# Kernel tuning notes

Measured on AMD Instinct MI355X. Metric: run time of the kernel, lower is better.

Reference implementation:

```python
import jax, jax.numpy as jnp
import numpy as np

N = 50000
NEG_SLOPE = 0.2  # PyG GATConv default leaky_relu slope


def _gat_layer(x, src, dst, W, a_s, a_d, b):
    # x: [N, Fin]; W: [Fin, H*C]; a_s, a_d: [H, C]; b: [C]
    H, C = a_s.shape
    xp = (x @ W).reshape(N, H, C)                      # projected node features per head
    alpha_s = jnp.einsum('nhc,hc->nh', xp, a_s)        # [N, H]
    alpha_d = jnp.einsum('nhc,hc->nh', xp, a_d)        # [N, H]
    e = jax.nn.leaky_relu(alpha_s[src] + alpha_d[dst], NEG_SLOPE)  # [E, H]
    # segment softmax over incoming edges of each dst node
    m = jax.ops.segment_max(e, dst, num_segments=N)
    m = jnp.where(jnp.isfinite(m), m, 0.0)
    p = jnp.exp(e - jax.lax.stop_gradient(m)[dst])
    denom = jax.ops.segment_sum(p, dst, num_segments=N)
    alpha = p / denom[dst]                             # [E, H]
    # scatter-aggregate messages
    out = jax.ops.segment_sum(alpha[:, :, None] * xp[src], dst, num_segments=N)  # [N, H, C]
    return out.mean(axis=1) + b                        # concat=False -> mean over heads


def setup_inputs() -> dict:
    key = jax.random.key(0)
    ks = jax.random.split(key, 16)
    IN, HID, OUT, H = 128, 64, 40, 4
    E = 800000
    x = jax.random.normal(ks[0], (N, IN), dtype=jnp.float32)
    edge_index = jax.random.randint(ks[1], (2, E), 0, N, dtype=jnp.int64)

    def mk(kw, ka, fin, fout):
        s = 1.0 / np.sqrt(fin)
        W = jax.random.normal(kw, (fin, H * fout), dtype=jnp.float32) * s
        a_s = jax.random.normal(ka, (H, fout), dtype=jnp.float32) * 0.1
        a_d = jax.random.normal(jax.random.fold_in(ka, 1), (H, fout), dtype=jnp.float32) * 0.1
        b = jnp.zeros((fout,), dtype=jnp.float32)
        return W, a_s, a_d, b

    W1, as1, ad1, b1 = mk(ks[2], ks[3], IN, HID)
    W2, as2, ad2, b2 = mk(ks[4], ks[5], HID, HID)
    W3, as3, ad3, b3 = mk(ks[6], ks[7], HID, OUT)
    return dict(x=x, edge_index=edge_index,
                W1=W1, as1=as1, ad1=ad1, b1=b1,
                W2=W2, as2=as2, ad2=ad2, b2=b2,
                W3=W3, as3=as3, ad3=ad3, b3=b3)


def reference(x, edge_index, W1, as1, ad1, b1, W2, as2, ad2, b2, W3, as3, ad3, b3):
    # PyG GATConv adds self-loops by default
    loop = jnp.arange(N, dtype=edge_index.dtype)
    src = jnp.concatenate([edge_index[0], loop])
    dst = jnp.concatenate([edge_index[1], loop])
    h = jax.nn.relu(_gat_layer(x, src, dst, W1, as1, ad1, b1))   # dropout is identity in eval
    h = jax.nn.relu(_gat_layer(h, src, dst, W2, as2, ad2, b2))
    h = jax.nn.relu(_gat_layer(h, src, dst, W3, as3, ad3, b3))
    return jax.nn.log_softmax(h, axis=-1)
```

## Files before the change

### kernel.cpp

```cpp
#include <hip/hip_runtime.h>
#include <math.h>

#define NNODES 50000
#define NEG_SLOPE 0.2f

typedef unsigned short ushort8v __attribute__((ext_vector_type(8)));
typedef unsigned short ushort4v __attribute__((ext_vector_type(4)));
typedef short short8v __attribute__((ext_vector_type(8)));
typedef float f32x4 __attribute__((ext_vector_type(4)));
typedef float f32x2 __attribute__((ext_vector_type(2)));

__device__ __forceinline__ unsigned short f2bf(float f){
    unsigned u = __float_as_uint(f);
    u += 0x7fff + ((u >> 16) & 1);
    return (unsigned short)(u >> 16);
}

__device__ __forceinline__ void emit_wa(const float* __restrict__ W, const float* __restrict__ a_s,
                                        const float* __restrict__ a_d, unsigned short* __restrict__ Wt,
                                        int Kin, int C, int id){
    const int n = id / Kin, k = id - n * Kin;
    float v = 0.f;
    if(n < 8){
        const int hh = n & 3;
        const float* av = (n < 4) ? a_s : a_d;
        for(int c = 0; c < C; c++) v += W[(size_t)k * (4 * C) + hh * C + c] * av[hh * C + c];
    }
    Wt[id] = f2bf(v);
}

__device__ __forceinline__ void emit_wc(const float* __restrict__ W, unsigned short* __restrict__ Wt,
                                        int Kin, int C, int id){
    const int c = id / (4 * Kin);
    const int hk = id - c * (4 * Kin);
    const int h = hk / Kin, k = hk - h * Kin;
    const float v = (c < C) ? W[(size_t)k * (4 * C) + h * C + c] * 0.25f : 0.f;
    Wt[id] = f2bf(v);
}

__global__ void initprep_kernel(const unsigned long long* __restrict__ e, int* __restrict__ flag,
                                int* __restrict__ deg, int N,
                                const float* __restrict__ x, unsigned short* __restrict__ xbf, int X4,
                                const float* __restrict__ W1, const float* __restrict__ as1, const float* __restrict__ ad1,
                                const float* __restrict__ W2, const float* __restrict__ as2, const float* __restrict__ ad2,
                                const float* __restrict__ W3, const float* __restrict__ as3, const float* __restrict__ ad3,
                                unsigned short* __restrict__ Wa1, unsigned short* __restrict__ Wa2,
                                unsigned short* __restrict__ Wa3, unsigned short* __restrict__ Wc1,
                                unsigned short* __restrict__ Wc2, unsigned short* __restrict__ Wc3){
    if(blockIdx.x == 0 && threadIdx.x < 64){
        const unsigned long long v = e[threadIdx.x];
        const unsigned long long mask = __ballot(v >= (1ULL << 32));
        if(threadIdx.x == 0) *flag = (mask == 0ULL) ? 1 : 0;
    }
    int id = blockIdx.x * blockDim.x + threadIdx.x;
    if(id < N) deg[id] = 0;
    if(id < X4){
        const float4 v = *(const float4*)&x[(size_t)id * 4];
        ushort4v o;
        o[0] = f2bf(v.x); o[1] = f2bf(v.y); o[2] = f2bf(v.z); o[3] = f2bf(v.w);
        *(ushort4v*)&xbf[(size_t)id * 4] = o;
        return;
    }
    id -= X4;
    if(id < 16 * 128){ emit_wa(W1, as1, ad1, Wa1, 128, 64, id); return; }
    id -= 16 * 128;
    if(id < 16 * 64){ emit_wa(W2, as2, ad2, Wa2, 64, 64, id); return; }
    id -= 16 * 64;
    if(id < 16 * 64){ emit_wa(W3, as3, ad3, Wa3, 64, 40, id); return; }
    id -= 16 * 64;
    if(id < 64 * 512){ emit_wc(W1, Wc1, 128, 64, id); return; }
    id -= 64 * 512;
    if(id < 64 * 256){ emit_wc(W2, Wc2, 64, 64, id); return; }
    id -= 64 * 256;
    if(id < 48 * 256){ emit_wc(W3, Wc3, 64, 40, id); }
}

__global__ void hist_kernel(const void* __restrict__ e, const int* __restrict__ flag,
                            int* __restrict__ deg, int E){
    const int i = blockIdx.x * blockDim.x + threadIdx.x;
    if(i < E){
        const int d = (*flag) ? (int)((const long long*)e)[E + i] : ((const int*)e)[E + i];
        atomicAdd(&deg[d], 1);
    }
}

__global__ __launch_bounds__(512) void scan1_kernel(const int* __restrict__ deg,
                                                    int* __restrict__ excl,
                                                    int* __restrict__ bsum, int n){
    __shared__ int sh[512];
    const int t = threadIdx.x;
    const int gid = blockIdx.x * 512 + t;
    const int v = (gid < n) ? deg[gid] : 0;
    sh[t] = v;
    __syncthreads();
    for(int off = 1; off < 512; off <<= 1){
        const int add = (t >= off) ? sh[t - off] : 0;
        __syncthreads();
        sh[t] += add;
        __syncthreads();
    }
    if(gid < n) excl[gid] = sh[t] - v;
    if(t == 511) bsum[blockIdx.x] = sh[511];
}

__global__ __launch_bounds__(128) void scan2_kernel(int* __restrict__ bsum, int nb){
    __shared__ int sh[128];
    const int t = threadIdx.x;
    const int v = (t < nb) ? bsum[t] : 0;
    sh[t] = v;
    __syncthreads();
    for(int off = 1; off < 128; off <<= 1){
        const int add = (t >= off) ? sh[t - off] : 0;
        __syncthreads();
        sh[t] += add;
        __syncthreads();
    }
    if(t < nb) bsum[t] = sh[t] - v;
}

__global__ void scan3_kernel(const int* __restrict__ excl, const int* __restrict__ bsum,
                             int* __restrict__ row_ptr, int* __restrict__ cursor,
                             int n, int E){
    const int gid = blockIdx.x * blockDim.x + threadIdx.x;
    if(gid < n){
        const int r = excl[gid] + bsum[gid >> 9];
        row_ptr[gid] = r;
        cursor[gid] = r;
    }
    if(gid == 0) row_ptr[n] = E;
}

__global__ void scatter_kernel(const void* __restrict__ e, const int* __restrict__ flag,
                               int* __restrict__ cursor, int* __restrict__ col, int E){
    const int i = blockIdx.x * blockDim.x + threadIdx.x;
    if(i < E){
        int s, d;
        if(*flag){ s = (int)((const long long*)e)[i]; d = (int)((const long long*)e)[E + i]; }
        else     { s = ((const int*)e)[i];            d = ((const int*)e)[E + i]; }
        const int pos = atomicAdd(&cursor[d], 1);
        col[pos] = s;
    }
}

template<int K>
__global__ __launch_bounds__(256) void agemm_kernel(const unsigned short* __restrict__ A,
                                                    const unsigned short* __restrict__ Wa,
                                                    float* __restrict__ ea, float* __restrict__ ed,
                                                    int M){
    const int lane = threadIdx.x & 63;
    const int wave = threadIdx.x >> 6;
    const int quad = lane >> 4;
    const int l16 = lane & 15;
    const int bm = blockIdx.x * 64;
    const int m = min(bm + wave * 16 + l16, M - 1);
    f32x4 acc = {0,0,0,0};
    #pragma unroll
    for(int k0 = 0; k0 < K; k0 += 32){
        const short8v a = *(const short8v*)&A[(size_t)m * K + k0 + quad * 8];
        const short8v b = *(const short8v*)&Wa[(size_t)l16 * K + k0 + quad * 8];
        acc = __builtin_amdgcn_mfma_f32_16x16x32_bf16(a, b, acc, 0, 0, 0);
    }
    if(l16 < 8){
        const int h = l16 & 3;
        float* dst = (l16 < 4) ? ea : ed;
        const int rbase = bm + wave * 16 + quad * 4;
        #pragma unroll
        for(int r = 0; r < 4; r++){
            const int row = rbase + r;
            if(row < M){
                const float v = acc[r];
                *(f32x2*)&dst[(size_t)row * 8 + 2 * h] = (f32x2){__expf(v), __expf(NEG_SLOPE * v)};
            }
        }
    }
}

template<int K, int NC, bool FINAL, bool ALPHA>
__global__ __launch_bounds__(256) void fused_kernel(const unsigned short* __restrict__ X,
                                                    const int* __restrict__ row_ptr,
                                                    const int* __restrict__ col,
                                                    const float* __restrict__ ea,
                                                    const float* __restrict__ ed,
                                                    const unsigned short* __restrict__ Bt,
                                                    const float* __restrict__ bias,
                                                    void* __restrict__ outv,
                                                    const unsigned short* __restrict__ Wa,
                                                    float* __restrict__ ea_o,
                                                    float* __restrict__ ed_o){
    constexpr int KC = 4 * K;
    constexpr int CPL = K / 16;
    constexpr int PAIRS = CPL / 2;
    constexpr int LSTR = KC + 8;
    __shared__ unsigned short lg[16][LSTR];
    __shared__ unsigned short lh[ALPHA ? 16 : 1][72];
    __shared__ float lo[FINAL ? 16 : 1][48];

    const int lane = threadIdx.x & 63;
    const int wave = threadIdx.x >> 6;
    const int slot = lane >> 4;
    const int pos  = lane & 15;
    const int nb   = blockIdx.x * 16;

    #pragma unroll 1
    for(int i = 0; i < 4; i++){
        const int row16 = wave * 4 + i;
        const int n = nb + row16;
        const int rs = row_ptr[n], re = row_ptr[n + 1];
        const int T = re - rs + 1;
        const float4 edA = *(const float4*)&ed[(size_t)n * 8];
        const float4 edB = *(const float4*)&ed[(size_t)n * 8 + 4];

        f32x2 acc[4][PAIRS];
        #pragma unroll
        for(int h = 0; h < 4; h++)
            #pragma unroll
            for(int p = 0; p < PAIRS; p++) acc[h][p] = (f32x2){0.f, 0.f};
        float dnm[4] = {0.f, 0.f, 0.f, 0.f};

        auto body = [&](int e){
            const int s = (e < re) ? col[e] : n;
            const float4 eaA = *(const float4*)&ea[(size_t)s * 8];
            const float4 eaB = *(const float4*)&ea[(size_t)s * 8 + 4];
            const float w0 = fmaxf(eaA.x * edA.x, eaA.y * edA.y);
            const float w1 = fmaxf(eaA.z * edA.z, eaA.w * edA.w);
            const float w2 = fmaxf(eaB.x * edB.x, eaB.y * edB.y);
            const float w3 = fmaxf(eaB.z * edB.z, eaB.w * edB.w);
            dnm[0] += w0; dnm[1] += w1; dnm[2] += w2; dnm[3] += w3;
            unsigned u[PAIRS];
            if constexpr(PAIRS == 2){
                const uint2 t2 = *(const uint2*)&X[(size_t)s * K + pos * CPL];
                u[0] = t2.x; u[1] = t2.y;
            } else {
                const uint4 t4 = *(const uint4*)&X[(size_t)s * K + pos * CPL];
                u[0] = t4.x; u[1] = t4.y; u[2] = t4.z; u[3] = t4.w;
            }
            #pragma unroll
            for(int p = 0; p < PAIRS; p++){
                const f32x2 v = {__uint_as_float(u[p] << 16), __uint_as_float(u[p] & 0xffff0000u)};
                acc[0][p] += (f32x2){w0, w0} * v;
                acc[1][p] += (f32x2){w1, w1} * v;
                acc[2][p] += (f32x2){w2, w2} * v;
                acc[3][p] += (f32x2){w3, w3} * v;
            }
        };

        int k = 0;
        for(; k + 8 <= T; k += 8){ body(rs + k + slot); body(rs + k + 4 + slot); }
        for(; k + 4 <= T; k += 4){ body(rs + k + slot); }
        if(k < T && slot < T - k){ body(rs + k + slot); }

        #pragma unroll
        for(int msk = 16; msk < 64; msk <<= 1){
            #pragma unroll
            for(int h = 0; h < 4; h++){
                #pragma unroll
                for(int p = 0; p < PAIRS; p++){
                    acc[h][p][0] += __shfl_xor(acc[h][p][0], msk);
                    acc[h][p][1] += __shfl_xor(acc[h][p][1], msk);
                }
                dnm[h] += __shfl_xor(dnm[h], msk);
            }
        }
        if(lane < 16){
            #pragma unroll
            for(int h = 0; h < 4; h++){
                const float sc = 1.f / dnm[h];
                if constexpr(PAIRS == 2){
                    ushort4v o;
                    o[0] = f2bf(acc[h][0][0] * sc); o[1] = f2bf(acc[h][0][1] * sc);
                    o[2] = f2bf(acc[h][1][0] * sc); o[3] = f2bf(acc[h][1][1] * sc);
                    *(ushort4v*)&lg[row16][h * K + pos * CPL] = o;
                } else {
                    ushort8v o;
                    #pragma unroll
                    for(int p = 0; p < 4; p++){
                        o[2*p]   = f2bf(acc[h][p][0] * sc);
                        o[2*p+1] = f2bf(acc[h][p][1] * sc);
                    }
                    *(ushort8v*)&lg[row16][h * K + pos * CPL] = o;
                }
            }
        }
    }
    __syncthreads();

    if constexpr(!FINAL){
        f32x4 acc4 = {0, 0, 0, 0};
        const int c = wave * 16 + pos;
        for(int k0 = 0; k0 < KC; k0 += 32){
            const short8v a = *(const short8v*)&lg[pos][k0 + slot * 8];
            const short8v b = *(const short8v*)&Bt[(size_t)c * KC + k0 + slot * 8];
            acc4 = __builtin_amdgcn_mfma_f32_16x16x32_bf16(a, b, acc4, 0, 0, 0);
        }
        unsigned short* out = (unsigned short*)outv;
        const float bc = bias[c];
        #pragma unroll
        for(int r = 0; r < 4; r++){
            const unsigned short hb = f2bf(fmaxf(acc4[r] + bc, 0.f));
            out[(size_t)(nb + slot * 4 + r) * NC + c] = hb;
            if constexpr(ALPHA) lh[slot * 4 + r][c] = hb;
        }
        if constexpr(ALPHA){
            __syncthreads();
            if(wave == 0){
                f32x4 a4 = {0, 0, 0, 0};
                #pragma unroll
                for(int k0 = 0; k0 < 64; k0 += 32){
                    const short8v a = *(const short8v*)&lh[pos][k0 + slot * 8];
                    const short8v b = *(const short8v*)&Wa[(size_t)pos * 64 + k0 + slot * 8];
                    a4 = __builtin_amdgcn_mfma_f32_16x16x32_bf16(a, b, a4, 0, 0, 0);
                }
                if(pos < 8){
                    const int h = pos & 3;
                    float* dst = (pos < 4) ? ea_o : ed_o;
                    #pragma unroll
                    for(int r = 0; r < 4; r++){
                        const int row = nb + slot * 4 + r;
                        const float v = a4[r];
                        *(f32x2*)&dst[(size_t)row * 8 + 2 * h] = (f32x2){__expf(v), __expf(NEG_SLOPE * v)};
                    }
                }
            }
        }
    } else {
        if(wave < 3){
            f32x4 acc4 = {0, 0, 0, 0};
            const int c = wave * 16 + pos;
            for(int k0 = 0; k0 < KC; k0 += 32){
                const short8v a = *(const short8v*)&lg[pos][k0 + slot * 8];
                const short8v b = *(const short8v*)&Bt[(size_t)c * KC + k0 + slot * 8];
                acc4 = __builtin_amdgcn_mfma_f32_16x16x32_bf16(a, b, acc4, 0, 0, 0);
            }
            const bool valid = c < 40;
            const float bc = valid ? bias[c] : 0.f;
            #pragma unroll
            for(int r = 0; r < 4; r++)
                lo[slot * 4 + r][c] = valid ? fmaxf(acc4[r] + bc, 0.f) : -INFINITY;
        }
        __syncthreads();
        const int r  = threadIdx.x >> 4;
        const int cc = threadIdx.x & 15;
        const float o0 = lo[r][cc];
        const float o1 = lo[r][cc + 16];
        const float o2 = lo[r][cc + 32];
        float mx = fmaxf(fmaxf(o0, o1), o2);
        #pragma unroll
        for(int off = 1; off < 16; off <<= 1) mx = fmaxf(mx, __shfl_xor(mx, off));
        float se = __expf(o0 - mx) + __expf(o1 - mx) + ((o2 > -INFINITY) ? __expf(o2 - mx) : 0.f);
        #pragma unroll
        for(int off = 1; off < 16; off <<= 1) se += __shfl_xor(se, off);
        const float lz = mx + logf(se);
        float* out = (float*)outv;
        const size_t rb = (size_t)(nb + r) * 40;
        out[rb + cc] = o0 - lz;
        out[rb + cc + 16] = o1 - lz;
        if(cc < 8) out[rb + cc + 32] = o2 - lz;
    }
}

extern "C" void kernel_launch(void* const* d_in, const int* in_sizes, int n_in,
                              void* d_out, int out_size, void* d_ws, size_t ws_size,
                              hipStream_t stream){
    const int N = NNODES;
    const int E = in_sizes[1] / 2;

    const float* x   = (const float*)d_in[0];
    const float* W1  = (const float*)d_in[2];
    const float* as1 = (const float*)d_in[3];
    const float* ad1 = (const float*)d_in[4];
    const float* b1  = (const float*)d_in[5];
    const float* W2  = (const float*)d_in[6];
    const float* as2 = (const float*)d_in[7];
    const float* ad2 = (const float*)d_in[8];
    const float* b2  = (const float*)d_in[9];
    const float* W3  = (const float*)d_in[10];
    const float* as3 = (const float*)d_in[11];
    const float* ad3 = (const float*)d_in[12];
    const float* b3  = (const float*)d_in[13];

    char* ws = (char*)d_ws;
    size_t off = 0;
    auto alloc = [&](size_t bytes) -> void* {
        void* p = ws + off;
        off = (off + bytes + 255) & ~(size_t)255;
        return p;
    };
    int*   flag    = (int*)  alloc(4);
    int*   row_ptr = (int*)  alloc((size_t)(N + 1) * 4);
    int*   colv    = (int*)  alloc((size_t)E * 4);
    int*   cursor  = (int*)  alloc((size_t)N * 4);
    int*   deg     = (int*)  alloc((size_t)N * 4);
    int*   excl    = (int*)  alloc((size_t)N * 4);
    int*   bsum    = (int*)  alloc(128 * 4);
    unsigned short* xbf = (unsigned short*)alloc((size_t)N * 128 * 2);
    unsigned short* Wa1 = (unsigned short*)alloc(16 * 128 * 2);
    unsigned short* Wa2 = (unsigned short*)alloc(16 * 64 * 2);
    unsigned short* Wa3 = (unsigned short*)alloc(16 * 64 * 2);
    unsigned short* Wc1 = (unsigned short*)alloc((size_t)64 * 512 * 2);
    unsigned short* Wc2 = (unsigned short*)alloc((size_t)64 * 256 * 2);
    unsigned short* Wc3 = (unsigned short*)alloc((size_t)48 * 256 * 2);
    float* eav0 = (float*)alloc((size_t)N * 8 * 4);
    float* edv0 = (float*)alloc((size_t)N * 8 * 4);
    float* eav1 = (float*)alloc((size_t)N * 8 * 4);
    float* edv1 = (float*)alloc((size_t)N * 8 * 4);
    unsigned short* h1  = (unsigned short*)alloc((size_t)N * 64 * 2);
    unsigned short* h2  = (unsigned short*)alloc((size_t)N * 64 * 2);
    (void)ws_size;

    const void* eraw = d_in[1];

    const int X4 = N * 128 / 4;
    const int prepTotal = X4 + 16*128 + 16*64 + 16*64 + 64*512 + 64*256 + 48*256;
    initprep_kernel<<<(prepTotal + 255) / 256, 256, 0, stream>>>(
        (const unsigned long long*)eraw, flag, deg, N, x, xbf, X4,
        W1, as1, ad1, W2, as2, ad2, W3, as3, ad3,
        Wa1, Wa2, Wa3, Wc1, Wc2, Wc3);

    hist_kernel<<<(E + 255) / 256, 256, 0, stream>>>(eraw, flag, deg, E);
    const int nbScan = (N + 511) / 512;
    scan1_kernel<<<nbScan, 512, 0, stream>>>(deg, excl, bsum, N);
    scan2_kernel<<<1, 128, 0, stream>>>(bsum, nbScan);
    scan3_kernel<<<(N + 255) / 256, 256, 0, stream>>>(excl, bsum, row_ptr, cursor, N, E);
    scatter_kernel<<<(E + 255) / 256, 256, 0, stream>>>(eraw, flag, cursor, colv, E);

    const int mBlocks = (N + 63) / 64;
    const int fBlocks = N / 16;

    agemm_kernel<128><<<mBlocks, 256, 0, stream>>>(xbf, Wa1, eav0, edv0, N);

    fused_kernel<128, 64, false, true><<<fBlocks, 256, 0, stream>>>(
        xbf, row_ptr, colv, eav0, edv0, Wc1, b1, h1, Wa2, eav1, edv1);

    fused_kernel<64, 64, false, true><<<fBlocks, 256, 0, stream>>>(
        h1, row_ptr, colv, eav1, edv1, Wc2, b2, h2, Wa3, eav0, edv0);

    fused_kernel<64, 40, true, false><<<fBlocks, 256, 0, stream>>>(
        h2, row_ptr, colv, eav0, edv0, Wc3, b3, d_out, nullptr, nullptr, nullptr);
}
```

Baseline: 419.3 us.

## Use 1024-thread blocks with one wave per node and split-K MFMA reduction

The fused GAT layer kernels move from 256-thread blocks, where each wave looped over four destination nodes, to 1024-thread blocks where each of 16 waves aggregates a single node. The dense projection that follows is split along K across four wave groups, and the partial MFMA results are summed through shared memory. The aim is more parallelism and latency hiding for the irregular neighbor gathers, and less serial GEMM work per wave. The cost is an extra barrier and shared-memory traffic, larger blocks that can limit occupancy under register pressure, and idle waves during the epilogues.

```diff
diff --git a/kernel.cpp b/kernel.cpp
--- a/kernel.cpp
+++ b/kernel.cpp
@@ -176,22 +176,25 @@
 }
 
 template<int K, int NC, bool FINAL, bool ALPHA>
-__global__ __launch_bounds__(256) void fused_kernel(const unsigned short* __restrict__ X,
-                                                    const int* __restrict__ row_ptr,
-                                                    const int* __restrict__ col,
-                                                    const float* __restrict__ ea,
-                                                    const float* __restrict__ ed,
-                                                    const unsigned short* __restrict__ Bt,
-                                                    const float* __restrict__ bias,
-                                                    void* __restrict__ outv,
-                                                    const unsigned short* __restrict__ Wa,
-                                                    float* __restrict__ ea_o,
-                                                    float* __restrict__ ed_o){
+__global__ __launch_bounds__(1024) void fused_kernel(const unsigned short* __restrict__ X,
+                                                     const int* __restrict__ row_ptr,
+                                                     const int* __restrict__ col,
+                                                     const float* __restrict__ ea,
+                                                     const float* __restrict__ ed,
+                                                     const unsigned short* __restrict__ Bt,
+                                                     const float* __restrict__ bias,
+                                                     void* __restrict__ outv,
+                                                     const unsigned short* __restrict__ Wa,
+                                                     float* __restrict__ ea_o,
+                                                     float* __restrict__ ed_o){
     constexpr int KC = 4 * K;
     constexpr int CPL = K / 16;
     constexpr int PAIRS = CPL / 2;
     constexpr int LSTR = KC + 8;
+    constexpr int NT = (NC + 15) / 16;
+    constexpr int KCH = KC / 4;
     __shared__ unsigned short lg[16][LSTR];
+    __shared__ float pt[3][NT][16][20];
     __shared__ unsigned short lh[ALPHA ? 16 : 1][72];
     __shared__ float lo[FINAL ? 16 : 1][48];
 
@@ -201,10 +204,8 @@
     const int pos  = lane & 15;
     const int nb   = blockIdx.x * 16;
 
-    #pragma unroll 1
-    for(int i = 0; i < 4; i++){
-        const int row16 = wave * 4 + i;
-        const int n = nb + row16;
+    {
+        const int n = nb + wave;
         const int rs = row_ptr[n], re = row_ptr[n + 1];
         const int T = re - rs + 1;
         const float4 edA = *(const float4*)&ed[(size_t)n * 8];
@@ -269,7 +270,7 @@
                     ushort4v o;
                     o[0] = f2bf(acc[h][0][0] * sc); o[1] = f2bf(acc[h][0][1] * sc);
                     o[2] = f2bf(acc[h][1][0] * sc); o[3] = f2bf(acc[h][1][1] * sc);
-                    *(ushort4v*)&lg[row16][h * K + pos * CPL] = o;
+                    *(ushort4v*)&lg[wave][h * K + pos * CPL] = o;
                 } else {
                     ushort8v o;
                     #pragma unroll
@@ -277,28 +278,47 @@
                         o[2*p]   = f2bf(acc[h][p][0] * sc);
                         o[2*p+1] = f2bf(acc[h][p][1] * sc);
                     }
-                    *(ushort8v*)&lg[row16][h * K + pos * CPL] = o;
+                    *(ushort8v*)&lg[wave][h * K + pos * CPL] = o;
                 }
             }
         }
     }
     __syncthreads();
 
-    if constexpr(!FINAL){
-        f32x4 acc4 = {0, 0, 0, 0};
-        const int c = wave * 16 + pos;
-        for(int k0 = 0; k0 < KC; k0 += 32){
+    const int t = wave & 3;
+    const int q = wave >> 2;
+    f32x4 acc4 = {0, 0, 0, 0};
+    if(t < NT){
+        const int c = t * 16 + pos;
+        const int kbeg = q * KCH;
+        #pragma unroll
+        for(int k0 = kbeg; k0 < kbeg + KCH; k0 += 32){
             const short8v a = *(const short8v*)&lg[pos][k0 + slot * 8];
             const short8v b = *(const short8v*)&Bt[(size_t)c * KC + k0 + slot * 8];
             acc4 = __builtin_amdgcn_mfma_f32_16x16x32_bf16(a, b, acc4, 0, 0, 0);
         }
-        unsigned short* out = (unsigned short*)outv;
-        const float bc = bias[c];
-        #pragma unroll
-        for(int r = 0; r < 4; r++){
-            const unsigned short hb = f2bf(fmaxf(acc4[r] + bc, 0.f));
-            out[(size_t)(nb + slot * 4 + r) * NC + c] = hb;
-            if constexpr(ALPHA) lh[slot * 4 + r][c] = hb;
+        if(q > 0){
+            #pragma unroll
+            for(int r = 0; r < 4; r++) pt[q - 1][t][slot * 4 + r][pos] = acc4[r];
+        }
+    }
+    __syncthreads();
+
+    if constexpr(!FINAL){
+        if(q == 0){
+            #pragma unroll
+            for(int r = 0; r < 4; r++)
+                acc4[r] += pt[0][t][slot * 4 + r][pos] + pt[1][t][slot * 4 + r][pos]
+                         + pt[2][t][slot * 4 + r][pos];
+            unsigned short* out = (unsigned short*)outv;
+            const int c = t * 16 + pos;
+            const float bc = bias[c];
+            #pragma unroll
+            for(int r = 0; r < 4; r++){
+                const unsigned short hb = f2bf(fmaxf(acc4[r] + bc, 0.f));
+                out[(size_t)(nb + slot * 4 + r) * NC + c] = hb;
+                if constexpr(ALPHA) lh[slot * 4 + r][c] = hb;
+            }
         }
         if constexpr(ALPHA){
             __syncthreads();
@@ -323,38 +343,36 @@
             }
         }
     } else {
-        if(wave < 3){
-            f32x4 acc4 = {0, 0, 0, 0};
-            const int c = wave * 16 + pos;
-            for(int k0 = 0; k0 < KC; k0 += 32){
-                const short8v a = *(const short8v*)&lg[pos][k0 + slot * 8];
-                const short8v b = *(const short8v*)&Bt[(size_t)c * KC + k0 + slot * 8];
-                acc4 = __builtin_amdgcn_mfma_f32_16x16x32_bf16(a, b, acc4, 0, 0, 0);
-            }
-            const bool valid = c < 40;
-            const float bc = valid ? bias[c] : 0.f;
-            #pragma unroll
-            for(int r = 0; r < 4; r++)
-                lo[slot * 4 + r][c] = valid ? fmaxf(acc4[r] + bc, 0.f) : -INFINITY;
+        if(q == 0 && t < NT){
+            #pragma unroll
+            for(int r = 0; r < 4; r++){
+                const float v = acc4[r] + pt[0][t][slot * 4 + r][pos]
+                              + pt[1][t][slot * 4 + r][pos] + pt[2][t][slot * 4 + r][pos];
+                const int c = t * 16 + pos;
+                const bool valid = c < 40;
+                lo[slot * 4 + r][c] = valid ? fmaxf(v + bias[c], 0.f) : -INFINITY;
+            }
         }
         __syncthreads();
-        const int r  = threadIdx.x >> 4;
-        const int cc = threadIdx.x & 15;
-        const float o0 = lo[r][cc];
-        const float o1 = lo[r][cc + 16];
-        const float o2 = lo[r][cc + 32];
-        float mx = fmaxf(fmaxf(o0, o1), o2);
-        #pragma unroll
-        for(int off = 1; off < 16; off <<= 1) mx = fmaxf(mx, __shfl_xor(mx, off));
-        float se = __expf(o0 - mx) + __expf(o1 - mx) + ((o2 > -INFINITY) ? __expf(o2 - mx) : 0.f);
-        #pragma unroll
-        for(int off = 1; off < 16; off <<= 1) se += __shfl_xor(se, off);
-        const float lz = mx + logf(se);
-        float* out = (float*)outv;
-        const size_t rb = (size_t)(nb + r) * 40;
-        out[rb + cc] = o0 - lz;
-        out[rb + cc + 16] = o1 - lz;
-        if(cc < 8) out[rb + cc + 32] = o2 - lz;
+        if(threadIdx.x < 256){
+            const int r  = threadIdx.x >> 4;
+            const int cc = threadIdx.x & 15;
+            const float o0 = lo[r][cc];
+            const float o1 = lo[r][cc + 16];
+            const float o2 = lo[r][cc + 32];
+            float mx = fmaxf(fmaxf(o0, o1), o2);
+            #pragma unroll
+            for(int off = 1; off < 16; off <<= 1) mx = fmaxf(mx, __shfl_xor(mx, off));
+            float se = __expf(o0 - mx) + __expf(o1 - mx) + ((o2 > -INFINITY) ? __expf(o2 - mx) : 0.f);
+            #pragma unroll
+            for(int off = 1; off < 16; off <<= 1) se += __shfl_xor(se, off);
+            const float lz = mx + logf(se);
+            float* out = (float*)outv;
+            const size_t rb = (size_t)(nb + r) * 40;
+            out[rb + cc] = o0 - lz;
+            out[rb + cc + 16] = o1 - lz;
+            if(cc < 8) out[rb + cc + 32] = o2 - lz;
+        }
     }
 }
 
@@ -428,12 +446,12 @@
 
     agemm_kernel<128><<<mBlocks, 256, 0, stream>>>(xbf, Wa1, eav0, edv0, N);
 
-    fused_kernel<128, 64, false, true><<<fBlocks, 256, 0, stream>>>(
+    fused_kernel<128, 64, false, true><<<fBlocks, 1024, 0, stream>>>(
         xbf, row_ptr, colv, eav0, edv0, Wc1, b1, h1, Wa2, eav1, edv1);
 
-    fused_kernel<64, 64, false, true><<<fBlocks, 256, 0, stream>>>(
+    fused_kernel<64, 64, false, true><<<fBlocks, 1024, 0, stream>>>(
         h1, row_ptr, colv, eav1, edv1, Wc2, b2, h2, Wa3, eav0, edv0);
 
-    fused_kernel<64, 40, true, false><<<fBlocks, 256, 0, stream>>>(
+    fused_kernel<64, 40, true, false><<<fBlocks, 1024, 0, stream>>>(
         h2, row_ptr, colv, eav0, edv0, Wc3, b3, d_out, nullptr, nullptr, nullptr);
 }
```

New measurement: 485.6 us. 1.16x slower.

## Precompute per-head projected features then aggregate with one-node-per-wave gather

Applied to the files above, without the earlier changes.

Replaces the aggregate-then-project fused kernel with a GEMM that materialises projected per-head features (plus attention logits) into a bf16 buffer, followed by a gather kernel where each wave handles one node and reads 256-wide projected rows per edge. Edge weights are computed once per edge and staged in LDS, then broadcast across lanes. This removes per-edge multi-head FMA work and the post-aggregation GEMM, but enlarges per-edge gather traffic and adds a write/read of an N×256 intermediate per layer.

```diff
diff --git a/kernel.cpp b/kernel.cpp
--- a/kernel.cpp
+++ b/kernel.cpp
@@ -16,25 +16,22 @@
     return (unsigned short)(u >> 16);
 }
 
-__device__ __forceinline__ void emit_wa(const float* __restrict__ W, const float* __restrict__ a_s,
-                                        const float* __restrict__ a_d, unsigned short* __restrict__ Wt,
-                                        int Kin, int C, int id){
-    const int n = id / Kin, k = id - n * Kin;
+__device__ __forceinline__ void emit_wpt(const float* __restrict__ W, const float* __restrict__ a_s,
+                                         const float* __restrict__ a_d, unsigned short* __restrict__ Wt,
+                                         int Kin, int C, int id){
+    const int j = id / Kin, k = id - j * Kin;
     float v = 0.f;
-    if(n < 8){
-        const int hh = n & 3;
-        const float* av = (n < 4) ? a_s : a_d;
-        for(int c = 0; c < C; c++) v += W[(size_t)k * (4 * C) + hh * C + c] * av[hh * C + c];
-    }
-    Wt[id] = f2bf(v);
-}
-
-__device__ __forceinline__ void emit_wc(const float* __restrict__ W, unsigned short* __restrict__ Wt,
-                                        int Kin, int C, int id){
-    const int c = id / (4 * Kin);
-    const int hk = id - c * (4 * Kin);
-    const int h = hk / Kin, k = hk - h * Kin;
-    const float v = (c < C) ? W[(size_t)k * (4 * C) + h * C + c] * 0.25f : 0.f;
+    if(j < 256){
+        const int h = j >> 6, c = j & 63;
+        v = (c < C) ? W[(size_t)k * (4 * C) + h * C + c] : 0.f;
+    } else {
+        const int n = j - 256;
+        if(n < 8){
+            const int hh = n & 3;
+            const float* av = (n < 4) ? a_s : a_d;
+            for(int c = 0; c < C; c++) v += W[(size_t)k * (4 * C) + hh * C + c] * av[hh * C + c];
+        }
+    }
     Wt[id] = f2bf(v);
 }
 
@@ -44,9 +41,8 @@
                                 const float* __restrict__ W1, const float* __restrict__ as1, const float* __restrict__ ad1,
                                 const float* __restrict__ W2, const float* __restrict__ as2, const float* __restrict__ ad2,
                                 const float* __restrict__ W3, const float* __restrict__ as3, const float* __restrict__ ad3,
-                                unsigned short* __restrict__ Wa1, unsigned short* __restrict__ Wa2,
-                                unsigned short* __restrict__ Wa3, unsigned short* __restrict__ Wc1,
-                                unsigned short* __restrict__ Wc2, unsigned short* __restrict__ Wc3){
+                                unsigned short* __restrict__ WpT1, unsigned short* __restrict__ WpT2,
+                                unsigned short* __restrict__ WpT3){
     if(blockIdx.x == 0 && threadIdx.x < 64){
         const unsigned long long v = e[threadIdx.x];
         const unsigned long long mask = __ballot(v >= (1ULL << 32));
@@ -62,17 +58,11 @@
         return;
     }
     id -= X4;
-    if(id < 16 * 128){ emit_wa(W1, as1, ad1, Wa1, 128, 64, id); return; }
-    id -= 16 * 128;
-    if(id < 16 * 64){ emit_wa(W2, as2, ad2, Wa2, 64, 64, id); return; }
-    id -= 16 * 64;
-    if(id < 16 * 64){ emit_wa(W3, as3, ad3, Wa3, 64, 40, id); return; }
-    id -= 16 * 64;
-    if(id < 64 * 512){ emit_wc(W1, Wc1, 128, 64, id); return; }
-    id -= 64 * 512;
-    if(id < 64 * 256){ emit_wc(W2, Wc2, 64, 64, id); return; }
-    id -= 64 * 256;
-    if(id < 48 * 256){ emit_wc(W3, Wc3, 64, 40, id); }
+    if(id < 272 * 128){ emit_wpt(W1, as1, ad1, WpT1, 128, 64, id); return; }
+    id -= 272 * 128;
+    if(id < 272 * 64){ emit_wpt(W2, as2, ad2, WpT2, 64, 64, id); return; }
+    id -= 272 * 64;
+    if(id < 272 * 64){ emit_wpt(W3, as3, ad3, WpT3, 64, 40, id); }
 }
 
 __global__ void hist_kernel(const void* __restrict__ e, const int* __restrict__ flag,
@@ -143,81 +133,82 @@
 }
 
 template<int K>
-__global__ __launch_bounds__(256) void agemm_kernel(const unsigned short* __restrict__ A,
-                                                    const unsigned short* __restrict__ Wa,
-                                                    float* __restrict__ ea, float* __restrict__ ed,
-                                                    int M){
+__global__ __launch_bounds__(256) void xpgemm_kernel(const unsigned short* __restrict__ A,
+                                                     const unsigned short* __restrict__ Bt,
+                                                     unsigned short* __restrict__ xp,
+                                                     float* __restrict__ ea, float* __restrict__ ed,
+                                                     int M){
+    constexpr int KK = K / 32;
     const int lane = threadIdx.x & 63;
     const int wave = threadIdx.x >> 6;
     const int quad = lane >> 4;
     const int l16 = lane & 15;
     const int bm = blockIdx.x * 64;
     const int m = min(bm + wave * 16 + l16, M - 1);
-    f32x4 acc = {0,0,0,0};
+    const int rbase = bm + wave * 16 + quad * 4;
+
+    short8v af[KK];
     #pragma unroll
-    for(int k0 = 0; k0 < K; k0 += 32){
-        const short8v a = *(const short8v*)&A[(size_t)m * K + k0 + quad * 8];
-        const short8v b = *(const short8v*)&Wa[(size_t)l16 * K + k0 + quad * 8];
-        acc = __builtin_amdgcn_mfma_f32_16x16x32_bf16(a, b, acc, 0, 0, 0);
-    }
-    if(l16 < 8){
-        const int h = l16 & 3;
-        float* dst = (l16 < 4) ? ea : ed;
-        const int rbase = bm + wave * 16 + quad * 4;
+    for(int kk = 0; kk < KK; kk++)
+        af[kk] = *(const short8v*)&A[(size_t)m * K + kk * 32 + quad * 8];
+
+    #pragma unroll
+    for(int t = 0; t < 17; t++){
+        f32x4 acc = {0, 0, 0, 0};
         #pragma unroll
-        for(int r = 0; r < 4; r++){
-            const int row = rbase + r;
-            if(row < M){
-                const float v = acc[r];
-                *(f32x2*)&dst[(size_t)row * 8 + 2 * h] = (f32x2){__expf(v), __expf(NEG_SLOPE * v)};
+        for(int kk = 0; kk < KK; kk++){
+            const short8v b = *(const short8v*)&Bt[(size_t)(t * 16 + l16) * K + kk * 32 + quad * 8];
+            acc = __builtin_amdgcn_mfma_f32_16x16x32_bf16(af[kk], b, acc, 0, 0, 0);
+        }
+        if(t < 16){
+            const int c = t * 16 + l16;
+            #pragma unroll
+            for(int r = 0; r < 4; r++){
+                const int row = rbase + r;
+                if(row < M) xp[(size_t)row * 256 + c] = f2bf(acc[r]);
             }
-        }
-    }
-}
-
-template<int K, int NC, bool FINAL, bool ALPHA>
-__global__ __launch_bounds__(256) void fused_kernel(const unsigned short* __restrict__ X,
-                                                    const int* __restrict__ row_ptr,
-                                                    const int* __restrict__ col,
-                                                    const float* __restrict__ ea,
-                                                    const float* __restrict__ ed,
-                                                    const unsigned short* __restrict__ Bt,
-                                                    const float* __restrict__ bias,
-                                                    void* __restrict__ outv,
-                                                    const unsigned short* __restrict__ Wa,
-                                                    float* __restrict__ ea_o,
-                                                    float* __restrict__ ed_o){
-    constexpr int KC = 4 * K;
-    constexpr int CPL = K / 16;
-    constexpr int PAIRS = CPL / 2;
-    constexpr int LSTR = KC + 8;
-    __shared__ unsigned short lg[16][LSTR];
-    __shared__ unsigned short lh[ALPHA ? 16 : 1][72];
-    __shared__ float lo[FINAL ? 16 : 1][48];
-
+        } else if(l16 < 8){
+            const int h = l16 & 3;
+            float* dst = (l16 < 4) ? ea : ed;
+            #pragma unroll
+            for(int r = 0; r < 4; r++){
+                const int row = rbase + r;
+                if(row < M){
+                    const float v = acc[r];
+                    *(f32x2*)&dst[(size_t)row * 8 + 2 * h] = (f32x2){__expf(v), __expf(NEG_SLOPE * v)};
+                }
+            }
+        }
+    }
+}
+
+template<bool FINAL>
+__global__ __launch_bounds__(256) void gatherp_kernel(const unsigned short* __restrict__ xp,
+                                                      const int* __restrict__ row_ptr,
+                                                      const int* __restrict__ col,
+                                                      const float* __restrict__ ea,
+                                                      const float* __restrict__ ed,
+                                                      const float* __restrict__ bias,
+                                                      void* __restrict__ outv){
+    __shared__ int   ls[4][64];
+    __shared__ float lw[4][64][4];
     const int lane = threadIdx.x & 63;
     const int wave = threadIdx.x >> 6;
-    const int slot = lane >> 4;
+    const int h    = lane >> 4;
     const int pos  = lane & 15;
-    const int nb   = blockIdx.x * 16;
-
-    #pragma unroll 1
-    for(int i = 0; i < 4; i++){
-        const int row16 = wave * 4 + i;
-        const int n = nb + row16;
-        const int rs = row_ptr[n], re = row_ptr[n + 1];
-        const int T = re - rs + 1;
-        const float4 edA = *(const float4*)&ed[(size_t)n * 8];
-        const float4 edB = *(const float4*)&ed[(size_t)n * 8 + 4];
-
-        f32x2 acc[4][PAIRS];
-        #pragma unroll
-        for(int h = 0; h < 4; h++)
-            #pragma unroll
-            for(int p = 0; p < PAIRS; p++) acc[h][p] = (f32x2){0.f, 0.f};
-        float dnm[4] = {0.f, 0.f, 0.f, 0.f};
-
-        auto body = [&](int e){
+    const int n    = blockIdx.x * 4 + wave;
+    const int rs = row_ptr[n], re = row_ptr[n + 1];
+    const int T = re - rs + 1;
+    const float4 edA = *(const float4*)&ed[(size_t)n * 8];
+    const float4 edB = *(const float4*)&ed[(size_t)n * 8 + 4];
+
+    float a0 = 0.f, a1 = 0.f, a2 = 0.f, a3 = 0.f;
+    float d0 = 0.f, d1 = 0.f, d2 = 0.f, d3 = 0.f;
+
+    for(int base = 0; base < T; base += 64){
+        const int ecnt = min(T - base, 64);
+        if(lane < ecnt){
+            const int e = rs + base + lane;
             const int s = (e < re) ? col[e] : n;
             const float4 eaA = *(const float4*)&ea[(size_t)s * 8];
             const float4 eaB = *(const float4*)&ea[(size_t)s * 8 + 4];
@@ -225,136 +216,71 @@
             const float w1 = fmaxf(eaA.z * edA.z, eaA.w * edA.w);
             const float w2 = fmaxf(eaB.x * edB.x, eaB.y * edB.y);
             const float w3 = fmaxf(eaB.z * edB.z, eaB.w * edB.w);
-            dnm[0] += w0; dnm[1] += w1; dnm[2] += w2; dnm[3] += w3;
-            unsigned u[PAIRS];
-            if constexpr(PAIRS == 2){
-                const uint2 t2 = *(const uint2*)&X[(size_t)s * K + pos * CPL];
-                u[0] = t2.x; u[1] = t2.y;
-            } else {
-                const uint4 t4 = *(const uint4*)&X[(size_t)s * K + pos * CPL];
-                u[0] = t4.x; u[1] = t4.y; u[2] = t4.z; u[3] = t4.w;
-            }
-            #pragma unroll
-            for(int p = 0; p < PAIRS; p++){
-                const f32x2 v = {__uint_as_float(u[p] << 16), __uint_as_float(u[p] & 0xffff0000u)};
-                acc[0][p] += (f32x2){w0, w0} * v;
-                acc[1][p] += (f32x2){w1, w1} * v;
-                acc[2][p] += (f32x2){w2, w2} * v;
-                acc[3][p] += (f32x2){w3, w3} * v;
-            }
+            d0 += w0; d1 += w1; d2 += w2; d3 += w3;
+            ls[wave][lane] = s;
+            *(f32x4*)&lw[wave][lane][0] = (f32x4){w0, w1, w2, w3};
+        }
+        auto body = [&](int e){
+            const int s   = ls[wave][e];
+            const float w = lw[wave][e][h];
+            const uint2 u = *(const uint2*)&xp[(size_t)s * 256 + lane * 4];
+            a0 += w * __uint_as_float(u.x << 16);
+            a1 += w * __uint_as_float(u.x & 0xffff0000u);
+            a2 += w * __uint_as_float(u.y << 16);
+            a3 += w * __uint_as_float(u.y & 0xffff0000u);
         };
-
-        int k = 0;
-        for(; k + 8 <= T; k += 8){ body(rs + k + slot); body(rs + k + 4 + slot); }
-        for(; k + 4 <= T; k += 4){ body(rs + k + slot); }
-        if(k < T && slot < T - k){ body(rs + k + slot); }
-
+        int e = 0;
+        for(; e + 4 <= ecnt; e += 4){ body(e); body(e + 1); body(e + 2); body(e + 3); }
+        for(; e < ecnt; e++) body(e);
+    }
+
+    #pragma unroll
+    for(int msk = 1; msk < 64; msk <<= 1){
+        d0 += __shfl_xor(d0, msk); d1 += __shfl_xor(d1, msk);
+        d2 += __shfl_xor(d2, msk); d3 += __shfl_xor(d3, msk);
+    }
+    const float dn = (h == 0) ? d0 : (h == 1) ? d1 : (h == 2) ? d2 : d3;
+    const float sc = 0.25f / dn;
+    a0 *= sc; a1 *= sc; a2 *= sc; a3 *= sc;
+    #pragma unroll
+    for(int msk = 16; msk < 64; msk <<= 1){
+        a0 += __shfl_xor(a0, msk); a1 += __shfl_xor(a1, msk);
+        a2 += __shfl_xor(a2, msk); a3 += __shfl_xor(a3, msk);
+    }
+    const int c0 = pos * 4;
+
+    if constexpr(!FINAL){
+        if(h == 0){
+            const float4 b4 = *(const float4*)&bias[c0];
+            unsigned short* out = (unsigned short*)outv;
+            ushort4v o;
+            o[0] = f2bf(fmaxf(a0 + b4.x, 0.f));
+            o[1] = f2bf(fmaxf(a1 + b4.y, 0.f));
+            o[2] = f2bf(fmaxf(a2 + b4.z, 0.f));
+            o[3] = f2bf(fmaxf(a3 + b4.w, 0.f));
+            *(ushort4v*)&out[(size_t)n * 64 + c0] = o;
+        }
+    } else {
+        float4 b4 = {0.f, 0.f, 0.f, 0.f};
+        if(c0 < 40) b4 = *(const float4*)&bias[c0];
+        const float o0 = (c0     < 40) ? fmaxf(a0 + b4.x, 0.f) : -INFINITY;
+        const float o1 = (c0 + 1 < 40) ? fmaxf(a1 + b4.y, 0.f) : -INFINITY;
+        const float o2 = (c0 + 2 < 40) ? fmaxf(a2 + b4.z, 0.f) : -INFINITY;
+        const float o3 = (c0 + 3 < 40) ? fmaxf(a3 + b4.w, 0.f) : -INFINITY;
+        float mx = fmaxf(fmaxf(o0, o1), fmaxf(o2, o3));
         #pragma unroll
-        for(int msk = 16; msk < 64; msk <<= 1){
-            #pragma unroll
-            for(int h = 0; h < 4; h++){
-                #pragma unroll
-                for(int p = 0; p < PAIRS; p++){
-                    acc[h][p][0] += __shfl_xor(acc[h][p][0], msk);
-                    acc[h][p][1] += __shfl_xor(acc[h][p][1], msk);
-                }
-                dnm[h] += __shfl_xor(dnm[h], msk);
-            }
-        }
-        if(lane < 16){
-            #pragma unroll
-            for(int h = 0; h < 4; h++){
-                const float sc = 1.f / dnm[h];
-                if constexpr(PAIRS == 2){
-                    ushort4v o;
-                    o[0] = f2bf(acc[h][0][0] * sc); o[1] = f2bf(acc[h][0][1] * sc);
-                    o[2] = f2bf(acc[h][1][0] * sc); o[3] = f2bf(acc[h][1][1] * sc);
-                    *(ushort4v*)&lg[row16][h * K + pos * CPL] = o;
-                } else {
-                    ushort8v o;
-                    #pragma unroll
-                    for(int p = 0; p < 4; p++){
-                        o[2*p]   = f2bf(acc[h][p][0] * sc);
-                        o[2*p+1] = f2bf(acc[h][p][1] * sc);
-                    }
-                    *(ushort8v*)&lg[row16][h * K + pos * CPL] = o;
-                }
-            }
-        }
-    }
-    __syncthreads();
-
-    if constexpr(!FINAL){
-        f32x4 acc4 = {0, 0, 0, 0};
-        const int c = wave * 16 + pos;
-        for(int k0 = 0; k0 < KC; k0 += 32){
-            const short8v a = *(const short8v*)&lg[pos][k0 + slot * 8];
-            const short8v b = *(const short8v*)&Bt[(size_t)c * KC + k0 + slot * 8];
-            acc4 = __builtin_amdgcn_mfma_f32_16x16x32_bf16(a, b, acc4, 0, 0, 0);
-        }
-        unsigned short* out = (unsigned short*)outv;
-        const float bc = bias[c];
+        for(int msk = 1; msk < 16; msk <<= 1) mx = fmaxf(mx, __shfl_xor(mx, msk));
+        float se = ((o0 > -INFINITY) ? __expf(o0 - mx) : 0.f)
+                 + ((o1 > -INFINITY) ? __expf(o1 - mx) : 0.f)
+                 + ((o2 > -INFINITY) ? __expf(o2 - mx) : 0.f)
+                 + ((o3 > -INFINITY) ? __expf(o3 - mx) : 0.f);
         #pragma unroll
-        for(int r = 0; r < 4; r++){
-            const unsigned short hb = f2bf(fmaxf(acc4[r] + bc, 0.f));
-            out[(size_t)(nb + slot * 4 + r) * NC + c] = hb;
-            if constexpr(ALPHA) lh[slot * 4 + r][c] = hb;
-        }
-        if constexpr(ALPHA){
-            __syncthreads();
-            if(wave == 0){
-                f32x4 a4 = {0, 0, 0, 0};
-                #pragma unroll
-                for(int k0 = 0; k0 < 64; k0 += 32){
-                    const short8v a = *(const short8v*)&lh[pos][k0 + slot * 8];
-                    const short8v b = *(const short8v*)&Wa[(size_t)pos * 64 + k0 + slot * 8];
-                    a4 = __builtin_amdgcn_mfma_f32_16x16x32_bf16(a, b, a4, 0, 0, 0);
-                }
-                if(pos < 8){
-                    const int h = pos & 3;
-                    float* dst = (pos < 4) ? ea_o : ed_o;
-                    #pragma unroll
-                    for(int r = 0; r < 4; r++){
-                        const int row = nb + slot * 4 + r;
-                        const float v = a4[r];
-                        *(f32x2*)&dst[(size_t)row * 8 + 2 * h] = (f32x2){__expf(v), __expf(NEG_SLOPE * v)};
-                    }
-                }
-            }
-        }
-    } else {
-        if(wave < 3){
-            f32x4 acc4 = {0, 0, 0, 0};
-            const int c = wave * 16 + pos;
-            for(int k0 = 0; k0 < KC; k0 += 32){
-                const short8v a = *(const short8v*)&lg[pos][k0 + slot * 8];
-                const short8v b = *(const short8v*)&Bt[(size_t)c * KC + k0 + slot * 8];
-                acc4 = __builtin_amdgcn_mfma_f32_16x16x32_bf16(a, b, acc4, 0, 0, 0);
-            }
-            const bool valid = c < 40;
-            const float bc = valid ? bias[c] : 0.f;
-            #pragma unroll
-            for(int r = 0; r < 4; r++)
-                lo[slot * 4 + r][c] = valid ? fmaxf(acc4[r] + bc, 0.f) : -INFINITY;
-        }
-        __syncthreads();
-        const int r  = threadIdx.x >> 4;
-        const int cc = threadIdx.x & 15;
-        const float o0 = lo[r][cc];
-        const float o1 = lo[r][cc + 16];
-        const float o2 = lo[r][cc + 32];
-        float mx = fmaxf(fmaxf(o0, o1), o2);
-        #pragma unroll
-        for(int off = 1; off < 16; off <<= 1) mx = fmaxf(mx, __shfl_xor(mx, off));
-        float se = __expf(o0 - mx) + __expf(o1 - mx) + ((o2 > -INFINITY) ? __expf(o2 - mx) : 0.f);
-        #pragma unroll
-        for(int off = 1; off < 16; off <<= 1) se += __shfl_xor(se, off);
+        for(int msk = 1; msk < 16; msk <<= 1) se += __shfl_xor(se, msk);
         const float lz = mx + logf(se);
-        float* out = (float*)outv;
-        const size_t rb = (size_t)(nb + r) * 40;
-        out[rb + cc] = o0 - lz;
-        out[rb + cc + 16] = o1 - lz;
-        if(cc < 8) out[rb + cc + 32] = o2 - lz;
+        if(h == 0 && c0 < 40){
+            float* out = (float*)outv;
+            *(f32x4*)&out[(size_t)n * 40 + c0] = (f32x4){o0 - lz, o1 - lz, o2 - lz, o3 - lz};
+        }
     }
 }
 
@@ -392,17 +318,13 @@
     int*   deg     = (int*)  alloc((size_t)N * 4);
     int*   excl    = (int*)  alloc((size_t)N * 4);
     int*   bsum    = (int*)  alloc(128 * 4);
-    unsigned short* xbf = (unsigned short*)alloc((size_t)N * 128 * 2);
-    unsigned short* Wa1 = (unsigned short*)alloc(16 * 128 * 2);
-    unsigned short* Wa2 = (unsigned short*)alloc(16 * 64 * 2);
-    unsigned short* Wa3 = (unsigned short*)alloc(16 * 64 * 2);
-    unsigned short* Wc1 = (unsigned short*)alloc((size_t)64 * 512 * 2);
-    unsigned short* Wc2 = (unsigned short*)alloc((size_t)64 * 256 * 2);
-    unsigned short* Wc3 = (unsigned short*)alloc((size_t)48 * 256 * 2);
-    float* eav0 = (float*)alloc((size_t)N * 8 * 4);
-    float* edv0 = (float*)alloc((size_t)N * 8 * 4);
-    float* eav1 = (float*)alloc((size_t)N * 8 * 4);
-    float* edv1 = (float*)alloc((size_t)N * 8 * 4);
+    unsigned short* xbf  = (unsigned short*)alloc((size_t)N * 128 * 2);
+    unsigned short* WpT1 = (unsigned short*)alloc((size_t)272 * 128 * 2);
+    unsigned short* WpT2 = (unsigned short*)alloc((size_t)272 * 64 * 2);
+    unsigned short* WpT3 = (unsigned short*)alloc((size_t)272 * 64 * 2);
+    float* eav = (float*)alloc((size_t)N * 8 * 4);
+    float* edv = (float*)alloc((size_t)N * 8 * 4);
+    unsigned short* xpv = (unsigned short*)alloc((size_t)N * 256 * 2);
     unsigned short* h1  = (unsigned short*)alloc((size_t)N * 64 * 2);
     unsigned short* h2  = (unsigned short*)alloc((size_t)N * 64 * 2);
     (void)ws_size;
@@ -410,11 +332,11 @@
     const void* eraw = d_in[1];
 
     const int X4 = N * 128 / 4;
-    const int prepTotal = X4 + 16*128 + 16*64 + 16*64 + 64*512 + 64*256 + 48*256;
+    const int prepTotal = X4 + 272 * 128 + 272 * 64 + 272 * 64;
     initprep_kernel<<<(prepTotal + 255) / 256, 256, 0, stream>>>(
         (const unsigned long long*)eraw, flag, deg, N, x, xbf, X4,
         W1, as1, ad1, W2, as2, ad2, W3, as3, ad3,
-        Wa1, Wa2, Wa3, Wc1, Wc2, Wc3);
+        WpT1, WpT2, WpT3);
 
     hist_kernel<<<(E + 255) / 256, 256, 0, stream>>>(eraw, flag, deg, E);
     const int nbScan = (N + 511) / 512;
@@ -424,16 +346,14 @@
     scatter_kernel<<<(E + 255) / 256, 256, 0, stream>>>(eraw, flag, cursor, colv, E);
 
     const int mBlocks = (N + 63) / 64;
-    const int fBlocks = N / 16;
-
-    agemm_kernel<128><<<mBlocks, 256, 0, stream>>>(xbf, Wa1, eav0, edv0, N);
-
-    fused_kernel<128, 64, false, true><<<fBlocks, 256, 0, stream>>>(
-        xbf, row_ptr, colv, eav0, edv0, Wc1, b1, h1, Wa2, eav1, edv1);
-
-    fused_kernel<64, 64, false, true><<<fBlocks, 256, 0, stream>>>(
-        h1, row_ptr, colv, eav1, edv1, Wc2, b2, h2, Wa3, eav0, edv0);
-
-    fused_kernel<64, 40, true, false><<<fBlocks, 256, 0, stream>>>(
-        h2, row_ptr, colv, eav0, edv0, Wc3, b3, d_out, nullptr, nullptr, nullptr);
-}
+    const int nodeBlocks = N / 4;
+
+    xpgemm_kernel<128><<<mBlocks, 256, 0, stream>>>(xbf, WpT1, xpv, eav, edv, N);
+    gatherp_kernel<false><<<nodeBlocks, 256, 0, stream>>>(xpv, row_ptr, colv, eav, edv, b1, h1);
+
+    xpgemm_kernel<64><<<mBlocks, 256, 0, stream>>>(h1, WpT2, xpv, eav, edv, N);
+    gatherp_kernel<false><<<nodeBlocks, 256, 0, stream>>>(xpv, row_ptr, colv, eav, edv, b2, h2);
+
+    xpgemm_kernel<64><<<mBlocks, 256, 0, stream>>>(h2, WpT3, xpv, eav, edv, N);
+    gatherp_kernel<true><<<nodeBlocks, 256, 0, stream>>>(xpv, row_ptr, colv, eav, edv, b3, d_out);
+}
```

Result: slower. 475.7 us (+13.4%).
